# Kernel optimization log

Measured on AMD Instinct MI355X. Metric: run time of the kernel, lower is better.

The kernel has to match this reference:

```python
import jax, jax.numpy as jnp
import numpy as np

# Dims: batch, seq, model dim, heads, routes-per-query, bleed-over alpha
B, S, D, H, K_ROUTES = 4, 512, 1024, 16, 64
HD = D // H                      # head_dim = 64
SCALE = 1.0 / float(np.sqrt(HD))
ALPHA = 0.25                     # neighbor bleed-over (forward arg default 0.0; >0 here)
CAUSAL = True
NEG = jnp.float32(-1e9)


def _build_routes(seq_len: int, k: int, depth: int = 8) -> np.ndarray:
    """Cantor-coordinate based positional routes (mirrors _build_positional_routes)."""
    pos = np.arange(seq_len, dtype=np.float64)
    x = pos / max(1, seq_len - 1)
    x = np.clip(x, 1e-6, 1.0 - 1e-6)
    val = np.zeros_like(x)
    factor = 0.5
    for _ in range(depth):
        xs = x * 3.0
        digit = xs.astype(np.int64)
        frac = xs - digit
        val = val + (digit == 2).astype(np.float64) * factor
        x = frac
        factor *= 0.5
    coords = np.clip(val, 0.0, 1.0)
    dist = np.abs(coords[:, None] - coords[None, :])            # [S,S]
    routes = np.argsort(dist, axis=1, kind='stable')[:, :k]     # k smallest distances
    return routes.astype(np.int32)


def setup_inputs() -> dict:
    key = jax.random.key(0)
    k0, k1, k2 = jax.random.split(key, 3)
    x = jax.random.normal(k0, (B, S, D), dtype=jnp.float32)
    # nn.Linear weights stored pre-transposed as [in, out] for clean matmul
    w_qkv = jax.random.normal(k1, (D, 3 * D), dtype=jnp.float32) * (1.0 / np.sqrt(D))
    b_qkv = jnp.zeros((3 * D,), dtype=jnp.float32)
    w_out = jax.random.normal(k2, (D, D), dtype=jnp.float32) * (1.0 / np.sqrt(D))
    b_out = jnp.zeros((D,), dtype=jnp.float32)
    routes = jnp.asarray(_build_routes(S, K_ROUTES), dtype=jnp.int32)  # [S, K]
    return {"x": x, "w_qkv": w_qkv, "b_qkv": b_qkv,
            "w_out": w_out, "b_out": b_out, "routes": routes}


def reference(x, w_qkv, b_qkv, w_out, b_out, routes):
    # QKV projection: [B,S,3D] -> [3,B,H,S,hd]
    qkv = (x @ w_qkv + b_qkv).reshape(B, S, 3, H, HD).transpose(2, 0, 3, 1, 4)
    q, k, v = qkv[0], qkv[1], qkv[2]                 # each [B,H,S,hd]

    r = routes                                        # [S,K]
    k_g = jnp.take(k, r, axis=2)                      # [B,H,S,K,hd]
    v_g = jnp.take(v, r, axis=2)
    if ALPHA > 0.0:
        rl = jnp.clip(r - 1, 0, S - 1)
        rr = jnp.clip(r + 1, 0, S - 1)
        k_g = (1.0 - ALPHA) * k_g + (ALPHA / 2.0) * (jnp.take(k, rl, axis=2) + jnp.take(k, rr, axis=2))
        v_g = (1.0 - ALPHA) * v_g + (ALPHA / 2.0) * (jnp.take(v, rl, axis=2) + jnp.take(v, rr, axis=2))

    scores = jnp.einsum('bhqd,bhqkd->bhqk', q, k_g) * SCALE   # [B,H,S,K]
    if CAUSAL:
        # route index > query position is masked (each query always routes to itself)
        mask = r > jnp.arange(S, dtype=r.dtype)[:, None]       # [S,K]
        scores = jnp.where(mask[None, None], NEG, scores)

    attn = jax.nn.softmax(scores, axis=-1)
    out = jnp.einsum('bhqk,bhqkd->bhqd', attn, v_g)            # [B,H,S,hd]
    out = out.transpose(0, 2, 1, 3).reshape(B, S, D)
    return out @ w_out + b_out
```

## Files before the change

### kernel.cpp

```cpp
#include <hip/hip_runtime.h>
#include <hip/hip_bf16.h>

#define BB 4
#define SS 512
#define DD 1024
#define HH 16
#define KR 64
#define HDIM 64
#define THREE_D 3072
#define M_ROWS 2048
#define SCALE_F 0.125f

typedef __attribute__((ext_vector_type(8))) short short8;
typedef __attribute__((ext_vector_type(4))) float floatx4;

union F8 { short8 s; unsigned int u[4]; unsigned short h[8]; };

__device__ inline float bfu(unsigned short h){ union{unsigned int u; float f;} c; c.u = ((unsigned int)h) << 16; return c.f; }
__device__ inline unsigned short f2bf(float f){
    union{float f; unsigned int u;} c; c.f = f;
    unsigned int u = c.u;
    return (unsigned short)((u + 0x7fffu + ((u >> 16) & 1u)) >> 16);
}

#define GLOAD_LDS16(g, l)                                                     \
    __builtin_amdgcn_global_load_lds(                                         \
        (const __attribute__((address_space(1))) unsigned int*)(g),           \
        (__attribute__((address_space(3))) unsigned int*)(l), 16, 0, 0)

__global__ __launch_bounds__(256) void prep_kernel(
    const float* __restrict__ x, const float* __restrict__ w_qkv,
    const float* __restrict__ w_out, const int* __restrict__ routes,
    unsigned short* __restrict__ xb_sw, unsigned short* __restrict__ wb1_sw,
    unsigned short* __restrict__ wb2_sw, unsigned int* __restrict__ maskg)
{
    const int bx = blockIdx.x;
    const int tid = threadIdx.x;
    if (bx < 1024) {
        int gid = bx * 256 + tid;
        int r  = gid & 127;
        int c  = (gid >> 7) & 3;
        int kt = (gid >> 9) & 31;
        int mt = gid >> 14;
        const float* src = x + ((size_t)(mt * 128 + r)) * 1024 + kt * 32 + c * 8;
        float4 a = *(const float4*)src;
        float4 b = *(const float4*)(src + 4);
        F8 o;
        o.h[0] = f2bf(a.x); o.h[1] = f2bf(a.y); o.h[2] = f2bf(a.z); o.h[3] = f2bf(a.w);
        o.h[4] = f2bf(b.x); o.h[5] = f2bf(b.y); o.h[6] = f2bf(b.z); o.h[7] = f2bf(b.w);
        *(uint4*)(xb_sw + (size_t)gid * 8) = *(uint4*)&o;
    } else if (bx < 3072) {
        const float* w;
        unsigned short* out;
        int gid, N;
        if (bx < 2560) { w = w_qkv; out = wb1_sw; N = THREE_D; gid = (bx - 1024) * 256 + tid; }
        else           { w = w_out; out = wb2_sw; N = DD;      gid = (bx - 2560) * 256 + tid; }
        int r  = gid & 127;
        int c  = (gid >> 7) & 3;
        int kt = (gid >> 9) & 31;
        int nt = gid >> 14;
        int n = nt * 128 + r;
        int kbase = kt * 32 + c * 8;
        F8 o;
#pragma unroll
        for (int j = 0; j < 8; ++j)
            o.h[j] = f2bf(w[(size_t)(kbase + j) * N + n]);
        *(uint4*)(out + (size_t)gid * 8) = *(uint4*)&o;
    } else {
        int q = (bx - 3072) * 256 + tid;
        unsigned int w[16];
#pragma unroll
        for (int i = 0; i < 16; ++i) w[i] = 0u;
        for (int j = 0; j < KR; ++j) {
            int r = routes[q * KR + j];
            if (r <= q) w[r >> 5] |= 1u << (r & 31);
        }
#pragma unroll
        for (int sw = 0; sw < 16; ++sw) maskg[sw * SS + q] = w[sw];
    }
}

__global__ __launch_bounds__(256) void gemm_qkv(
    const unsigned short* __restrict__ Asw,
    const unsigned short* __restrict__ Bsw,
    const float* __restrict__ bias,
    unsigned short* __restrict__ qb, unsigned short* __restrict__ kb,
    unsigned short* __restrict__ vb)
{
    __shared__ __align__(16) unsigned short Sh[12288];
    unsigned short* Alds = Sh;
    unsigned short* Blds = Sh + 4096;

    const int tid  = threadIdx.x;
    const int lane = tid & 63;
    const int wid  = tid >> 6;
    const int l15  = lane & 15;
    const int quad = lane >> 4;

    const int bid  = blockIdx.x;
    const int xcd  = bid & 7;
    const int loc  = bid >> 3;
    const int mt64 = (xcd & 3) * 8 + (loc & 7);
    const int nt   = (xcd >> 2) * 12 + (loc >> 3);

    const int mt = mt64 >> 1;
    const int rh = (mt64 & 1) * 64;
    const int wn = wid * 32;

    floatx4 acc[4][2];
#pragma unroll
    for (int i = 0; i < 4; ++i)
#pragma unroll
        for (int j = 0; j < 2; ++j) acc[i][j] = (floatx4){0.f, 0.f, 0.f, 0.f};

    for (int kt2 = 0; kt2 < 16; ++kt2) {
#pragma unroll
        for (int kh = 0; kh < 2; ++kh) {
            int kt = kt2 * 2 + kh;
            const unsigned short* ga = Asw + ((size_t)(mt * 32 + kt) * 4 + wid) * 1024 + (rh + lane) * 8;
            const unsigned short* gb = Bsw + (size_t)(nt * 32 + kt) * 4096 + wid * 1024 + lane * 8;
            GLOAD_LDS16(ga,       Alds + kh * 2048 + wid * 512 + lane * 8);
            GLOAD_LDS16(gb,       Blds + kh * 4096 + wid * 1024 + lane * 8);
            GLOAD_LDS16(gb + 512, Blds + kh * 4096 + wid * 1024 + 512 + lane * 8);
        }
        __syncthreads();

#pragma unroll
        for (int kh = 0; kh < 2; ++kh) {
            F8 af[4], bf[2];
#pragma unroll
            for (int mi = 0; mi < 4; ++mi)
                af[mi] = *(const F8*)(Alds + kh * 2048 + (size_t)(quad * 64 + mi * 16 + l15) * 8);
#pragma unroll
            for (int ni = 0; ni < 2; ++ni)
                bf[ni] = *(const F8*)(Blds + kh * 4096 + (size_t)(quad * 128 + wn + ni * 16 + l15) * 8);
#pragma unroll
            for (int mi = 0; mi < 4; ++mi)
#pragma unroll
                for (int ni = 0; ni < 2; ++ni)
                    acc[mi][ni] = __builtin_amdgcn_mfma_f32_16x16x32_bf16(
                        af[mi].s, bf[ni].s, acc[mi][ni], 0, 0, 0);
        }
        __syncthreads();
    }

    const int m0 = mt64 * 64;
    const int n0 = nt * 128;

#pragma unroll
    for (int mi = 0; mi < 4; ++mi) {
#pragma unroll
        for (int ni = 0; ni < 2; ++ni) {
            int col = wn + ni * 16 + l15;
            float bv = bias[n0 + col];
#pragma unroll
            for (int r = 0; r < 4; ++r) {
                int row = mi * 16 + quad * 4 + r;
                Sh[row * 136 + col] = f2bf(acc[mi][ni][r] + bv);
            }
        }
    }
    __syncthreads();

    for (int i = tid; i < 1024; i += 256) {
        int rr = i >> 4, cc = i & 15;
        int grow = m0 + rr, gcol = n0 + cc * 8;
        int b = grow >> 9, s = grow & 511;
        int which = gcol >> 10, rem = gcol & 1023;
        int h = rem >> 6, hd = rem & 63;
        unsigned short* dst = (which == 0) ? qb : (which == 1) ? kb : vb;
        uint4 val = *(const uint4*)(Sh + rr * 136 + cc * 8);
        *(uint4*)(dst + (((size_t)(b * HH + h) * SS) + s) * HDIM + hd) = val;
    }
}

__global__ __launch_bounds__(256) void gemm_out(
    const unsigned short* __restrict__ Asw,
    const unsigned short* __restrict__ Bsw,
    const float* __restrict__ bias,
    float* __restrict__ Cout)
{
    __shared__ __align__(16) unsigned short Alds[4096];
    __shared__ __align__(16) unsigned short Blds[4096];

    const int tid  = threadIdx.x;
    const int lane = tid & 63;
    const int wid  = tid >> 6;
    const int l15  = lane & 15;
    const int quad = lane >> 4;

    const int bid  = blockIdx.x;
    const int xcd  = bid & 7;
    const int loc  = bid >> 3;
    const int mt64 = (xcd & 3) * 8 + (loc & 7);
    const int nt64 = (xcd >> 2) * 8 + (loc >> 3);

    const int mt  = mt64 >> 1;
    const int rh  = (mt64 & 1) * 64;
    const int ntB = nt64 >> 1;
    const int rhB = (nt64 & 1) * 64;
    const int wm  = (wid >> 1) * 32;
    const int wn  = (wid & 1) * 32;

    floatx4 acc[2][2];
#pragma unroll
    for (int i = 0; i < 2; ++i)
#pragma unroll
        for (int j = 0; j < 2; ++j) acc[i][j] = (floatx4){0.f, 0.f, 0.f, 0.f};

    for (int kt2 = 0; kt2 < 16; ++kt2) {
#pragma unroll
        for (int kh = 0; kh < 2; ++kh) {
            int kt = kt2 * 2 + kh;
            const unsigned short* ga = Asw + ((size_t)(mt  * 32 + kt) * 4 + wid) * 1024 + (rh  + lane) * 8;
            const unsigned short* gb = Bsw + ((size_t)(ntB * 32 + kt) * 4 + wid) * 1024 + (rhB + lane) * 8;
            GLOAD_LDS16(ga, Alds + kh * 2048 + wid * 512 + lane * 8);
            GLOAD_LDS16(gb, Blds + kh * 2048 + wid * 512 + lane * 8);
        }
        __syncthreads();

#pragma unroll
        for (int kh = 0; kh < 2; ++kh) {
            F8 af[2], bf[2];
#pragma unroll
            for (int mi = 0; mi < 2; ++mi)
                af[mi] = *(const F8*)(Alds + kh * 2048 + (size_t)(quad * 64 + wm + mi * 16 + l15) * 8);
#pragma unroll
            for (int ni = 0; ni < 2; ++ni)
                bf[ni] = *(const F8*)(Blds + kh * 2048 + (size_t)(quad * 64 + wn + ni * 16 + l15) * 8);
#pragma unroll
            for (int mi = 0; mi < 2; ++mi)
#pragma unroll
                for (int ni = 0; ni < 2; ++ni)
                    acc[mi][ni] = __builtin_amdgcn_mfma_f32_16x16x32_bf16(
                        af[mi].s, bf[ni].s, acc[mi][ni], 0, 0, 0);
        }
        __syncthreads();
    }

    const int m0 = mt64 * 64;
    const int n0 = nt64 * 64;
#pragma unroll
    for (int mi = 0; mi < 2; ++mi) {
#pragma unroll
        for (int ni = 0; ni < 2; ++ni) {
            int col = n0 + wn + ni * 16 + l15;
            float bv = bias[col];
#pragma unroll
            for (int r = 0; r < 4; ++r) {
                int row = m0 + wm + mi * 16 + quad * 4 + r;
                Cout[(size_t)row * DD + col] = acc[mi][ni][r] + bv;
            }
        }
    }
}

__global__ __launch_bounds__(256) void blend_v_kernel(
    const unsigned short* __restrict__ vb, unsigned short* __restrict__ Vtg)
{
    __shared__ float vt[130][65];
    const int bh = blockIdx.x >> 2;
    const int sb = (blockIdx.x & 3) * 128;
    const int tid = threadIdx.x;
    const unsigned short* vbase = vb + (size_t)bh * SS * HDIM;

    for (int i = tid; i < 130 * 8; i += 256) {
        int row = i >> 3, c8 = (i & 7) << 3;
        int s = sb + row - 1; s = s < 0 ? 0 : (s > SS - 1 ? SS - 1 : s);
        F8 vv = *(const F8*)(vbase + (size_t)s * 64 + c8);
#pragma unroll
        for (int j = 0; j < 8; ++j) vt[row][c8 + j] = bfu(vv.h[j]);
    }
    __syncthreads();

    for (int i = tid; i < 64 * 32; i += 256) {
        int d = i >> 5, s4 = (i & 31) << 2;
        ushort4 o;
        o.x = f2bf(0.75f * vt[s4+1][d] + 0.125f * (vt[s4+0][d] + vt[s4+2][d]));
        o.y = f2bf(0.75f * vt[s4+2][d] + 0.125f * (vt[s4+1][d] + vt[s4+3][d]));
        o.z = f2bf(0.75f * vt[s4+3][d] + 0.125f * (vt[s4+2][d] + vt[s4+4][d]));
        o.w = f2bf(0.75f * vt[s4+4][d] + 0.125f * (vt[s4+3][d] + vt[s4+5][d]));
        *(ushort4*)(Vtg + ((size_t)bh * 64 + d) * SS + sb + s4) = o;
    }
}

__global__ __launch_bounds__(512, 2) void attn_kernel(
    const unsigned short* __restrict__ qb,
    const unsigned short* __restrict__ kbuf,
    const unsigned short* __restrict__ Vtg,
    const unsigned int* __restrict__ maskg,
    unsigned short* __restrict__ attn_sw)
{
    __shared__ __align__(16) unsigned short Ks[512 * 64];
    __shared__ __align__(16) unsigned short Vs[64 * 512];
    __shared__ __align__(16) unsigned short Ps[8 * 16 * 64];

    const int bh = blockIdx.x >> 2;
    const int qt = blockIdx.x & 3;
    const int b = bh >> 4, h = bh & 15;
    const int tid  = threadIdx.x;
    const int lane = tid & 63;
    const int wid  = tid >> 6;
    const int l15  = lane & 15;
    const int quad = lane >> 4;

    {
        const unsigned short* kbh = kbuf + (size_t)bh * (SS * 64);
        uint4* dst = (uint4*)Ks;
        for (int c = tid; c < 4096; c += 512) {
            int s = c >> 3, cc = c & 7;
            int sm = s ? s - 1 : 0;
            int sp = (s < SS - 1) ? s + 1 : SS - 1;
            F8 k0 = *(const F8*)(kbh + (size_t)s  * 64 + cc * 8);
            F8 km = *(const F8*)(kbh + (size_t)sm * 64 + cc * 8);
            F8 kp = *(const F8*)(kbh + (size_t)sp * 64 + cc * 8);
            F8 o;
#pragma unroll
            for (int j = 0; j < 8; ++j)
                o.h[j] = f2bf(0.75f * bfu(k0.h[j]) + 0.125f * (bfu(km.h[j]) + bfu(kp.h[j])));
            dst[(s << 3) | (cc ^ (s & 7))] = *(uint4*)&o;
        }
        const uint4* srcv = (const uint4*)(Vtg + (size_t)bh * (64 * SS));
        uint4* dstv = (uint4*)Vs;
        for (int c = tid; c < 4096; c += 512) {
            int d = c >> 6, sc = c & 63;
            dstv[(d << 6) | (sc & 56) | ((sc ^ d) & 7)] = srcv[c];
        }
    }
    __syncthreads();

    const int qbase = qt * 128 + wid * 16;
    const int q = qbase + l15;

    F8 qf[2];
    {
        const unsigned short* qrow = qb + ((size_t)bh * SS + q) * 64;
        qf[0] = *(const F8*)(qrow + quad * 8);
        qf[1] = *(const F8*)(qrow + 32 + quad * 8);
    }

    floatx4 accS[32];
#pragma unroll
    for (int st = 0; st < 32; ++st) {
        int srow = st * 16 + l15;
        const F8 k0 = *(const F8*)(Ks + (((srow << 3) | ( quad      ^ (srow & 7))) << 3));
        const F8 k1 = *(const F8*)(Ks + (((srow << 3) | ((4 + quad) ^ (srow & 7))) << 3));
        floatx4 a = (floatx4){0.f, 0.f, 0.f, 0.f};
        a = __builtin_amdgcn_mfma_f32_16x16x32_bf16(k0.s, qf[0].s, a, 0, 0, 0);
        a = __builtin_amdgcn_mfma_f32_16x16x32_bf16(k1.s, qf[1].s, a, 0, 0, 0);
        accS[st] = a;
    }

    floatx4 accO[4];
#pragma unroll
    for (int dt = 0; dt < 4; ++dt) accO[dt] = (floatx4){0.f, 0.f, 0.f, 0.f};
    float lsum = 0.f;
    unsigned int* Pw = (unsigned int*)Ps + wid * 512;

#pragma unroll
    for (int ch = 0; ch < 8; ++ch) {
        unsigned int mw0 = maskg[(ch * 2) * SS + q];
        unsigned int mw1 = maskg[(ch * 2 + 1) * SS + q];
#pragma unroll
        for (int t = 0; t < 4; ++t) {
            unsigned int mw = (t & 2) ? mw1 : mw0;
            int sbase = (t & 1) * 16 + quad * 4;
            floatx4 a = accS[ch * 4 + t];
            float e0 = ((mw >> (sbase + 0)) & 1u) ? __expf(a[0] * SCALE_F) : 0.f;
            float e1 = ((mw >> (sbase + 1)) & 1u) ? __expf(a[1] * SCALE_F) : 0.f;
            float e2 = ((mw >> (sbase + 2)) & 1u) ? __expf(a[2] * SCALE_F) : 0.f;
            float e3 = ((mw >> (sbase + 3)) & 1u) ? __expf(a[3] * SCALE_F) : 0.f;
            lsum += (e0 + e1) + (e2 + e3);
            unsigned int w0 = (unsigned int)f2bf(e0) | ((unsigned int)f2bf(e1) << 16);
            unsigned int w1 = (unsigned int)f2bf(e2) | ((unsigned int)f2bf(e3) << 16);
            int off0 = t * 8 + quad * 2;
            int off1 = off0 + 1;
            Pw[l15 * 32 + ((((off0 >> 2) ^ (l15 & 7)) << 2) | (off0 & 3))] = w0;
            Pw[l15 * 32 + ((((off1 >> 2) ^ (l15 & 7)) << 2) | (off1 & 3))] = w1;
        }
        F8 pa[2];
#pragma unroll
        for (int ks = 0; ks < 2; ++ks) {
            int ci = ks * 4 + quad;
            pa[ks] = *(const F8*)((const unsigned short*)(Pw + l15 * 32) +
                                  ((ci ^ (l15 & 7)) << 3));
        }
#pragma unroll
        for (int dt = 0; dt < 4; ++dt) {
            int d = dt * 16 + l15;
#pragma unroll
            for (int ks = 0; ks < 2; ++ks) {
                int sc = ch * 8 + ks * 4 + quad;
                const F8 bv = *(const F8*)(Vs + (((d << 6) | (sc & 56) | ((sc ^ d) & 7)) << 3));
                accO[dt] = __builtin_amdgcn_mfma_f32_16x16x32_bf16(pa[ks].s, bv.s, accO[dt], 0, 0, 0);
            }
        }
    }

    lsum += __shfl_xor(lsum, 16);
    lsum += __shfl_xor(lsum, 32);
    float inv = 1.0f / lsum;

    unsigned short* Ow = Ps + wid * 1024;
#pragma unroll
    for (int r = 0; r < 4; ++r) {
        float invr = __shfl(inv, quad * 4 + r);
#pragma unroll
        for (int dt = 0; dt < 4; ++dt)
            Ow[(quad * 4 + r) * 64 + dt * 16 + l15] = f2bf(accO[dt][r] * invr);
    }
#pragma unroll
    for (int i = 0; i < 2; ++i) {
        int ch = i * 64 + lane;
        int qlocal = ch >> 3, j = ch & 7;
        int qq = qt * 128 + wid * 16 + qlocal;
        int mrow = b * SS + qq;
        int mt = mrow >> 7, rr = mrow & 127;
        int kt2 = h * 2 + (j >> 2), c = j & 3;
        size_t gid = (((size_t)(mt * 32 + kt2) * 4 + c) * 128 + rr);
        *(uint4*)(attn_sw + gid * 8) = *(const uint4*)(Ow + qlocal * 64 + j * 8);
    }
}

extern "C" void kernel_launch(void* const* d_in, const int* in_sizes, int n_in,
                              void* d_out, int out_size, void* d_ws, size_t ws_size,
                              hipStream_t stream)
{
    const float* x     = (const float*)d_in[0];
    const float* w_qkv = (const float*)d_in[1];
    const float* b_qkv = (const float*)d_in[2];
    const float* w_out = (const float*)d_in[3];
    const float* b_out = (const float*)d_in[4];
    const int* routes  = (const int*)d_in[5];

    char* w = (char*)d_ws;
    unsigned short* xb_sw  = (unsigned short*)(w);
    unsigned short* wb1_sw = (unsigned short*)(w + (4u  << 20));
    unsigned short* wb2_sw = (unsigned short*)(w + (10u << 20));
    unsigned short* qbuf   = (unsigned short*)(w + (12u << 20));
    unsigned short* kbuf   = (unsigned short*)(w + (16u << 20));
    unsigned short* vbuf   = (unsigned short*)(w + (20u << 20));
    unsigned short* Vtg    = (unsigned short*)(w + (24u << 20));
    unsigned short* attnsw = (unsigned short*)(w + (28u << 20));
    unsigned int*   maskg  = (unsigned int*)(w + (32u << 20));

    prep_kernel<<<3074, 256, 0, stream>>>(x, w_qkv, w_out, routes,
                                          xb_sw, wb1_sw, wb2_sw, maskg);

    gemm_qkv<<<768, 256, 0, stream>>>(xb_sw, wb1_sw, b_qkv, qbuf, kbuf, vbuf);

    blend_v_kernel<<<256, 256, 0, stream>>>(vbuf, Vtg);

    attn_kernel<<<256, 512, 0, stream>>>(qbuf, kbuf, Vtg, maskg, attnsw);

    gemm_out<<<512, 256, 0, stream>>>(attnsw, wb2_sw, b_out, (float*)d_out);
}
```

Measured before the change: 148.1 us.

## Precompute blended K in blend kernel and double-buffer K/V chunks in attention

The K neighbor blend moves out of the attention kernel into the blend kernel, which now writes pre-swizzled K and V quarter-chunks to global memory. The attention kernel streams these chunks into double-buffered LDS with direct global-to-LDS loads, overlapping each chunk's load with compute on the previous one and cutting score registers from 32 to 8 tiles. This removes 256 redundant per-block K blends and the serialized full-sequence load, but adds an extra global round trip for blended K and a barrier per chunk.

```diff
diff --git a/kernel.cpp b/kernel.cpp
--- a/kernel.cpp
+++ b/kernel.cpp
@@ -255,45 +255,67 @@
     }
 }
 
-__global__ __launch_bounds__(256) void blend_v_kernel(
-    const unsigned short* __restrict__ vb, unsigned short* __restrict__ Vtg)
+__global__ __launch_bounds__(256) void blend_kv_kernel(
+    const unsigned short* __restrict__ kb, const unsigned short* __restrict__ vb,
+    unsigned short* __restrict__ K2g, unsigned short* __restrict__ Vtg)
 {
     __shared__ float vt[130][65];
     const int bh = blockIdx.x >> 2;
-    const int sb = (blockIdx.x & 3) * 128;
+    const int qd = blockIdx.x & 3;
+    const int s0 = qd * 128;
     const int tid = threadIdx.x;
+    const unsigned short* kbase = kb + (size_t)bh * SS * HDIM;
     const unsigned short* vbase = vb + (size_t)bh * SS * HDIM;
+    unsigned short* Kq = K2g + ((size_t)(bh * 4 + qd)) * 8192;
+    unsigned short* Vq = Vtg + ((size_t)(bh * 4 + qd)) * 8192;
 
     for (int i = tid; i < 130 * 8; i += 256) {
         int row = i >> 3, c8 = (i & 7) << 3;
-        int s = sb + row - 1; s = s < 0 ? 0 : (s > SS - 1 ? SS - 1 : s);
+        int s = s0 + row - 1; s = s < 0 ? 0 : (s > SS - 1 ? SS - 1 : s);
         F8 vv = *(const F8*)(vbase + (size_t)s * 64 + c8);
 #pragma unroll
         for (int j = 0; j < 8; ++j) vt[row][c8 + j] = bfu(vv.h[j]);
     }
+
+    for (int i = tid; i < 1024; i += 256) {
+        int sl = i >> 3, cc = i & 7;
+        int s = s0 + sl;
+        int sm = s ? s - 1 : 0;
+        int sp = (s < SS - 1) ? s + 1 : SS - 1;
+        F8 k0 = *(const F8*)(kbase + (size_t)s  * 64 + cc * 8);
+        F8 km = *(const F8*)(kbase + (size_t)sm * 64 + cc * 8);
+        F8 kp = *(const F8*)(kbase + (size_t)sp * 64 + cc * 8);
+        F8 o;
+#pragma unroll
+        for (int j = 0; j < 8; ++j)
+            o.h[j] = f2bf(0.75f * bfu(k0.h[j]) + 0.125f * (bfu(km.h[j]) + bfu(kp.h[j])));
+        *(uint4*)(Kq + (size_t)(sl * 8 + (cc ^ (sl & 7))) * 8) = *(uint4*)&o;
+    }
     __syncthreads();
 
-    for (int i = tid; i < 64 * 32; i += 256) {
-        int d = i >> 5, s4 = (i & 31) << 2;
-        ushort4 o;
-        o.x = f2bf(0.75f * vt[s4+1][d] + 0.125f * (vt[s4+0][d] + vt[s4+2][d]));
-        o.y = f2bf(0.75f * vt[s4+2][d] + 0.125f * (vt[s4+1][d] + vt[s4+3][d]));
-        o.z = f2bf(0.75f * vt[s4+3][d] + 0.125f * (vt[s4+2][d] + vt[s4+4][d]));
-        o.w = f2bf(0.75f * vt[s4+4][d] + 0.125f * (vt[s4+3][d] + vt[s4+5][d]));
-        *(ushort4*)(Vtg + ((size_t)bh * 64 + d) * SS + sb + s4) = o;
-    }
-}
-
-__global__ __launch_bounds__(512, 2) void attn_kernel(
+    for (int i = tid; i < 1024; i += 256) {
+        int d = i >> 4, scl = i & 15;
+        F8 o;
+#pragma unroll
+        for (int a = 0; a < 8; ++a) {
+            int rl = scl * 8 + a;
+            o.h[a] = f2bf(0.75f * vt[rl + 1][d] + 0.125f * (vt[rl][d] + vt[rl + 2][d]));
+        }
+        int chunk = d * 16 + (scl & 8) + ((scl ^ d) & 7);
+        *(uint4*)(Vq + (size_t)chunk * 8) = *(uint4*)&o;
+    }
+}
+
+__global__ __launch_bounds__(512) void attn_kernel(
     const unsigned short* __restrict__ qb,
-    const unsigned short* __restrict__ kbuf,
+    const unsigned short* __restrict__ K2g,
     const unsigned short* __restrict__ Vtg,
     const unsigned int* __restrict__ maskg,
     unsigned short* __restrict__ attn_sw)
 {
-    __shared__ __align__(16) unsigned short Ks[512 * 64];
-    __shared__ __align__(16) unsigned short Vs[64 * 512];
-    __shared__ __align__(16) unsigned short Ps[8 * 16 * 64];
+    __shared__ __align__(16) unsigned short Ks2[2][8192];
+    __shared__ __align__(16) unsigned short Vs2[2][8192];
+    __shared__ __align__(16) unsigned short Ps[8192];
 
     const int bh = blockIdx.x >> 2;
     const int qt = blockIdx.x & 3;
@@ -304,30 +326,17 @@
     const int l15  = lane & 15;
     const int quad = lane >> 4;
 
-    {
-        const unsigned short* kbh = kbuf + (size_t)bh * (SS * 64);
-        uint4* dst = (uint4*)Ks;
-        for (int c = tid; c < 4096; c += 512) {
-            int s = c >> 3, cc = c & 7;
-            int sm = s ? s - 1 : 0;
-            int sp = (s < SS - 1) ? s + 1 : SS - 1;
-            F8 k0 = *(const F8*)(kbh + (size_t)s  * 64 + cc * 8);
-            F8 km = *(const F8*)(kbh + (size_t)sm * 64 + cc * 8);
-            F8 kp = *(const F8*)(kbh + (size_t)sp * 64 + cc * 8);
-            F8 o;
-#pragma unroll
-            for (int j = 0; j < 8; ++j)
-                o.h[j] = f2bf(0.75f * bfu(k0.h[j]) + 0.125f * (bfu(km.h[j]) + bfu(kp.h[j])));
-            dst[(s << 3) | (cc ^ (s & 7))] = *(uint4*)&o;
-        }
-        const uint4* srcv = (const uint4*)(Vtg + (size_t)bh * (64 * SS));
-        uint4* dstv = (uint4*)Vs;
-        for (int c = tid; c < 4096; c += 512) {
-            int d = c >> 6, sc = c & 63;
-            dstv[(d << 6) | (sc & 56) | ((sc ^ d) & 7)] = srcv[c];
-        }
-    }
-    __syncthreads();
+    const unsigned short* Kbh = K2g + (size_t)bh * 4 * 8192;
+    const unsigned short* Vbh = Vtg + (size_t)bh * 4 * 8192;
+
+    #define STAGE(qd, bufi) do {                                              \
+        const unsigned short* kq = Kbh + (size_t)(qd) * 8192;                 \
+        const unsigned short* vq = Vbh + (size_t)(qd) * 8192;                 \
+        GLOAD_LDS16(kq + wid * 1024 + lane * 8,       Ks2[bufi] + wid * 1024 + lane * 8);        \
+        GLOAD_LDS16(kq + wid * 1024 + 512 + lane * 8, Ks2[bufi] + wid * 1024 + 512 + lane * 8);  \
+        GLOAD_LDS16(vq + wid * 1024 + lane * 8,       Vs2[bufi] + wid * 1024 + lane * 8);        \
+        GLOAD_LDS16(vq + wid * 1024 + 512 + lane * 8, Vs2[bufi] + wid * 1024 + 512 + lane * 8);  \
+    } while (0)
 
     const int qbase = qt * 128 + wid * 16;
     const int q = qbase + l15;
@@ -339,17 +348,8 @@
         qf[1] = *(const F8*)(qrow + 32 + quad * 8);
     }
 
-    floatx4 accS[32];
-#pragma unroll
-    for (int st = 0; st < 32; ++st) {
-        int srow = st * 16 + l15;
-        const F8 k0 = *(const F8*)(Ks + (((srow << 3) | ( quad      ^ (srow & 7))) << 3));
-        const F8 k1 = *(const F8*)(Ks + (((srow << 3) | ((4 + quad) ^ (srow & 7))) << 3));
-        floatx4 a = (floatx4){0.f, 0.f, 0.f, 0.f};
-        a = __builtin_amdgcn_mfma_f32_16x16x32_bf16(k0.s, qf[0].s, a, 0, 0, 0);
-        a = __builtin_amdgcn_mfma_f32_16x16x32_bf16(k1.s, qf[1].s, a, 0, 0, 0);
-        accS[st] = a;
-    }
+    STAGE(0, 0);
+    __syncthreads();
 
     floatx4 accO[4];
 #pragma unroll
@@ -357,44 +357,64 @@
     float lsum = 0.f;
     unsigned int* Pw = (unsigned int*)Ps + wid * 512;
 
-#pragma unroll
-    for (int ch = 0; ch < 8; ++ch) {
-        unsigned int mw0 = maskg[(ch * 2) * SS + q];
-        unsigned int mw1 = maskg[(ch * 2 + 1) * SS + q];
-#pragma unroll
-        for (int t = 0; t < 4; ++t) {
-            unsigned int mw = (t & 2) ? mw1 : mw0;
-            int sbase = (t & 1) * 16 + quad * 4;
-            floatx4 a = accS[ch * 4 + t];
-            float e0 = ((mw >> (sbase + 0)) & 1u) ? __expf(a[0] * SCALE_F) : 0.f;
-            float e1 = ((mw >> (sbase + 1)) & 1u) ? __expf(a[1] * SCALE_F) : 0.f;
-            float e2 = ((mw >> (sbase + 2)) & 1u) ? __expf(a[2] * SCALE_F) : 0.f;
-            float e3 = ((mw >> (sbase + 3)) & 1u) ? __expf(a[3] * SCALE_F) : 0.f;
-            lsum += (e0 + e1) + (e2 + e3);
-            unsigned int w0 = (unsigned int)f2bf(e0) | ((unsigned int)f2bf(e1) << 16);
-            unsigned int w1 = (unsigned int)f2bf(e2) | ((unsigned int)f2bf(e3) << 16);
-            int off0 = t * 8 + quad * 2;
-            int off1 = off0 + 1;
-            Pw[l15 * 32 + ((((off0 >> 2) ^ (l15 & 7)) << 2) | (off0 & 3))] = w0;
-            Pw[l15 * 32 + ((((off1 >> 2) ^ (l15 & 7)) << 2) | (off1 & 3))] = w1;
-        }
-        F8 pa[2];
-#pragma unroll
-        for (int ks = 0; ks < 2; ++ks) {
-            int ci = ks * 4 + quad;
-            pa[ks] = *(const F8*)((const unsigned short*)(Pw + l15 * 32) +
-                                  ((ci ^ (l15 & 7)) << 3));
-        }
-#pragma unroll
-        for (int dt = 0; dt < 4; ++dt) {
-            int d = dt * 16 + l15;
+    for (int qd = 0; qd < 4; ++qd) {
+        if (qd < 3) STAGE(qd + 1, (qd + 1) & 1);
+        const unsigned short* Ksb = Ks2[qd & 1];
+        const unsigned short* Vsb = Vs2[qd & 1];
+
+        floatx4 accS[8];
+#pragma unroll
+        for (int st = 0; st < 8; ++st) {
+            int srow = st * 16 + l15;
+            const F8 k0 = *(const F8*)(Ksb + (((srow << 3) | ( quad      ^ (srow & 7))) << 3));
+            const F8 k1 = *(const F8*)(Ksb + (((srow << 3) | ((4 + quad) ^ (srow & 7))) << 3));
+            floatx4 a = (floatx4){0.f, 0.f, 0.f, 0.f};
+            a = __builtin_amdgcn_mfma_f32_16x16x32_bf16(k0.s, qf[0].s, a, 0, 0, 0);
+            a = __builtin_amdgcn_mfma_f32_16x16x32_bf16(k1.s, qf[1].s, a, 0, 0, 0);
+            accS[st] = a;
+        }
+
+#pragma unroll
+        for (int ch2 = 0; ch2 < 2; ++ch2) {
+            unsigned int mw0 = maskg[(qd * 4 + ch2 * 2) * SS + q];
+            unsigned int mw1 = maskg[(qd * 4 + ch2 * 2 + 1) * SS + q];
+#pragma unroll
+            for (int t = 0; t < 4; ++t) {
+                unsigned int mw = (t & 2) ? mw1 : mw0;
+                int sbase = (t & 1) * 16 + quad * 4;
+                floatx4 a = accS[ch2 * 4 + t];
+                float e0 = ((mw >> (sbase + 0)) & 1u) ? __expf(a[0] * SCALE_F) : 0.f;
+                float e1 = ((mw >> (sbase + 1)) & 1u) ? __expf(a[1] * SCALE_F) : 0.f;
+                float e2 = ((mw >> (sbase + 2)) & 1u) ? __expf(a[2] * SCALE_F) : 0.f;
+                float e3 = ((mw >> (sbase + 3)) & 1u) ? __expf(a[3] * SCALE_F) : 0.f;
+                lsum += (e0 + e1) + (e2 + e3);
+                unsigned int w0 = (unsigned int)f2bf(e0) | ((unsigned int)f2bf(e1) << 16);
+                unsigned int w1 = (unsigned int)f2bf(e2) | ((unsigned int)f2bf(e3) << 16);
+                int off0 = t * 8 + quad * 2;
+                int off1 = off0 + 1;
+                Pw[l15 * 32 + ((((off0 >> 2) ^ (l15 & 7)) << 2) | (off0 & 3))] = w0;
+                Pw[l15 * 32 + ((((off1 >> 2) ^ (l15 & 7)) << 2) | (off1 & 3))] = w1;
+            }
+            F8 pa[2];
 #pragma unroll
             for (int ks = 0; ks < 2; ++ks) {
-                int sc = ch * 8 + ks * 4 + quad;
-                const F8 bv = *(const F8*)(Vs + (((d << 6) | (sc & 56) | ((sc ^ d) & 7)) << 3));
-                accO[dt] = __builtin_amdgcn_mfma_f32_16x16x32_bf16(pa[ks].s, bv.s, accO[dt], 0, 0, 0);
+                int ci = ks * 4 + quad;
+                pa[ks] = *(const F8*)((const unsigned short*)(Pw + l15 * 32) +
+                                      ((ci ^ (l15 & 7)) << 3));
             }
-        }
+#pragma unroll
+            for (int dt = 0; dt < 4; ++dt) {
+                int d = dt * 16 + l15;
+#pragma unroll
+                for (int ks = 0; ks < 2; ++ks) {
+                    int scl = ch2 * 8 + ks * 4 + quad;
+                    int chunk = d * 16 + (scl & 8) + ((scl ^ d) & 7);
+                    const F8 bv = *(const F8*)(Vsb + ((size_t)chunk << 3));
+                    accO[dt] = __builtin_amdgcn_mfma_f32_16x16x32_bf16(pa[ks].s, bv.s, accO[dt], 0, 0, 0);
+                }
+            }
+        }
+        __syncthreads();
     }
 
     lsum += __shfl_xor(lsum, 16);
@@ -420,6 +440,7 @@
         size_t gid = (((size_t)(mt * 32 + kt2) * 4 + c) * 128 + rr);
         *(uint4*)(attn_sw + gid * 8) = *(const uint4*)(Ow + qlocal * 64 + j * 8);
     }
+    #undef STAGE
 }
 
 extern "C" void kernel_launch(void* const* d_in, const int* in_sizes, int n_in,
@@ -440,18 +461,19 @@
     unsigned short* qbuf   = (unsigned short*)(w + (12u << 20));
     unsigned short* kbuf   = (unsigned short*)(w + (16u << 20));
     unsigned short* vbuf   = (unsigned short*)(w + (20u << 20));
-    unsigned short* Vtg    = (unsigned short*)(w + (24u << 20));
-    unsigned short* attnsw = (unsigned short*)(w + (28u << 20));
-    unsigned int*   maskg  = (unsigned int*)(w + (32u << 20));
+    unsigned short* K2g    = (unsigned short*)(w + (24u << 20));
+    unsigned short* Vtg    = (unsigned short*)(w + (28u << 20));
+    unsigned short* attnsw = (unsigned short*)(w + (32u << 20));
+    unsigned int*   maskg  = (unsigned int*)(w + (36u << 20));
 
     prep_kernel<<<3074, 256, 0, stream>>>(x, w_qkv, w_out, routes,
                                           xb_sw, wb1_sw, wb2_sw, maskg);
 
     gemm_qkv<<<768, 256, 0, stream>>>(xb_sw, wb1_sw, b_qkv, qbuf, kbuf, vbuf);
 
-    blend_v_kernel<<<256, 256, 0, stream>>>(vbuf, Vtg);
-
-    attn_kernel<<<256, 512, 0, stream>>>(qbuf, kbuf, Vtg, maskg, attnsw);
+    blend_kv_kernel<<<256, 256, 0, stream>>>(kbuf, vbuf, K2g, Vtg);
+
+    attn_kernel<<<256, 512, 0, stream>>>(qbuf, K2g, Vtg, maskg, attnsw);
 
     gemm_out<<<512, 256, 0, stream>>>(attnsw, wb2_sw, b_out, (float*)d_out);
 }
```

Result: no change. 145.4 us (-1.8%).
